# Kernel tuning notes

Hardware: AMD Instinct MI355X
Metric: run time of the kernel (lower is better)

## Reference

```python
import jax, jax.numpy as jnp
import numpy as np

NV, NH = 6000, 6000
DV, DH = 1024, 1024
HID, HEADS = 128, 3
EV, EH, EC = 200000, 200000, 32768


def _gat(x, ei, W, a_src, a_dst, bias, edge_attr=None, lin_e=None, a_e=None):
    """PyG GATConv (heads=H, concat=False, add_self_loops=True, LeakyReLU 0.2).
    Returns (node_out [N,C], alpha [E+N, H])."""
    N = x.shape[0]
    H, C = a_src.shape
    xw = (x @ W).reshape(N, H, C)                      # [N,H,C]
    asrc = jnp.einsum('nhc,hc->nh', xw, a_src)         # [N,H]
    adst = jnp.einsum('nhc,hc->nh', xw, a_dst)
    loop = jnp.arange(N, dtype=ei.dtype)               # self-loops appended
    src = jnp.concatenate([ei[0], loop])
    dst = jnp.concatenate([ei[1], loop])
    alpha = asrc[src] + adst[dst]                      # [E+N,H]
    if edge_attr is not None:
        # edge_dim=1 path: lin_edge(weight)[E,H,C] dotted with att_edge; self-loop attr = mean (PyG fill_value='mean')
        ea = jnp.concatenate([edge_attr, jnp.full((N,), jnp.mean(edge_attr), edge_attr.dtype)])
        ef = (ea[:, None] * lin_e[None, :]).reshape(-1, H, C)
        alpha = alpha + jnp.einsum('ehc,hc->eh', ef, a_e)
    alpha = jax.nn.leaky_relu(alpha, 0.2)
    # segment softmax over incoming edges of each destination node
    amax = jax.ops.segment_max(alpha, dst, num_segments=N)
    ex = jnp.exp(alpha - amax[dst])
    den = jax.ops.segment_sum(ex, dst, num_segments=N)
    alpha = ex / (den[dst] + 1e-16)
    out = jax.ops.segment_sum(xw[src] * alpha[..., None], dst, num_segments=N)
    return out.mean(axis=1) + bias, alpha              # concat=False -> head mean


def _bn(x, g, b):  # BatchNorm1d, training mode (batch stats, biased var)
    m = x.mean(0)
    v = x.var(0)
    return (x - m) / jnp.sqrt(v + 1e-5) * g + b


def reference(virus_data, host_data, coexistence_data, virus_edge_weight, host_edge_weight,
              vW, v_asrc, v_adst, v_bias, v_line, v_atte,
              hW, h_asrc, h_adst, h_bias, h_line, h_atte,
              vhW, vh_asrc, vh_adst, vh_bias,
              hvW, hv_asrc, hv_adst, hv_bias,
              linv_W, linv_b, linh_W, linh_b, bn_g, bn_b,
              virus_edge_index, host_edge_index, coexistence_edge_index, coexistence_edge_index_t):
    feat_v, alpha_v = _gat(virus_data, virus_edge_index, vW, v_asrc, v_adst, v_bias,
                           virus_edge_weight, v_line, v_atte)
    feat_h, alpha_h = _gat(host_data, host_edge_index, hW, h_asrc, h_adst, h_bias,
                           host_edge_weight, h_line, h_atte)
    feat_vh, alpha_vh = _gat(coexistence_data, coexistence_edge_index_t, vhW, vh_asrc, vh_adst, vh_bias)
    feat_hv, alpha_hv = _gat(coexistence_data.T, coexistence_edge_index, hvW, hv_asrc, hv_adst, hv_bias)

    vh = jax.nn.leaky_relu(_bn(virus_data @ linv_W + linv_b, bn_g, bn_b), 0.01)
    hh = jax.nn.leaky_relu(_bn(host_data @ linh_W + linh_b, bn_g, bn_b), 0.01)

    output_host = vh @ hh.T                  # [Nv,Nh]
    output_virus = (hh @ vh.T).T             # [Nv,Nh]
    return (output_host, output_virus, output_host + output_virus,
            alpha_v, alpha_h, alpha_vh, alpha_hv,
            feat_v, feat_h, feat_vh, feat_hv)


def setup_inputs() -> dict:
    key = jax.random.key(0)
    ks = iter(jax.random.split(key, 48))

    def nrm(shape, s=0.05):
        return (jax.random.normal(next(ks), shape, jnp.float32) * s).astype(jnp.float32)

    def gat_params(din, edge=True):
        p = [nrm((din, HEADS * HID)), nrm((HEADS, HID)), nrm((HEADS, HID)), jnp.zeros((HID,), jnp.float32)]
        if edge:
            p += [nrm((HEADS * HID,)), nrm((HEADS, HID))]
        return p

    inp = {
        'virus_data': jax.random.normal(next(ks), (NV, DV), jnp.float32),
        'host_data': jax.random.normal(next(ks), (NH, DH), jnp.float32),
        'coexistence_data': jax.random.normal(next(ks), (DV, DH), jnp.float32),
        'virus_edge_weight': jax.random.uniform(next(ks), (EV,), jnp.float32),
        'host_edge_weight': jax.random.uniform(next(ks), (EH,), jnp.float32),
    }
    for pref, din, edge in [('v', DV, True), ('h', DH, True)]:
        W, asrc, adst, b, le, ae = gat_params(din, True)
        inp.update({f'{pref}W': W, f'{pref}_asrc': asrc, f'{pref}_adst': adst,
                    f'{pref}_bias': b, f'{pref}_line': le, f'{pref}_atte': ae})
    for pref, din in [('vh', DH), ('hv', DV)]:
        W, asrc, adst, b = gat_params(din, False)
        inp.update({f'{pref}W': W, f'{pref}_asrc': asrc, f'{pref}_adst': adst, f'{pref}_bias': b})
    inp.update({
        'linv_W': nrm((DV, HID)), 'linv_b': jnp.zeros((HID,), jnp.float32),
        'linh_W': nrm((DH, HID)), 'linh_b': jnp.zeros((HID,), jnp.float32),
        'bn_g': jnp.ones((HID,), jnp.float32), 'bn_b': jnp.zeros((HID,), jnp.float32),
        'virus_edge_index': jax.random.randint(next(ks), (2, EV), 0, NV, jnp.int32),
        'host_edge_index': jax.random.randint(next(ks), (2, EH), 0, NH, jnp.int32),
        'coexistence_edge_index': jax.random.randint(next(ks), (2, EC), 0, DH, jnp.int32),
        'coexistence_edge_index_t': jax.random.randint(next(ks), (2, EC), 0, DV, jnp.int32),
    })
    return inp
```

## Files before the change

### kernel.cpp

```cpp
#include <hip/hip_runtime.h>

#define NV   6000
#define NH   6000
#define EV   200000
#define EH   200000
#define EC   32768
#define GCAP 256

typedef __attribute__((ext_vector_type(8))) short bf16x8;
typedef __attribute__((ext_vector_type(4))) float f32x4;

__device__ __forceinline__ unsigned short f2bf(float f){
  unsigned u = __float_as_uint(f);
  u += 0x7FFFu + ((u >> 16) & 1u);
  return (unsigned short)(u >> 16);
}
__device__ __forceinline__ float bf2f(unsigned short h){
  return __uint_as_float((unsigned)h << 16);
}

__global__ __launch_bounds__(256) void k_prep(
    const float* __restrict__ virus, const float* __restrict__ hostd, const float* __restrict__ coex,
    const float* __restrict__ vW, const float* __restrict__ linvW,
    const float* __restrict__ hW, const float* __restrict__ linhW,
    const float* __restrict__ vhW, const float* __restrict__ hvW,
    const float* __restrict__ v_as, const float* __restrict__ v_ad,
    const float* __restrict__ h_as, const float* __restrict__ h_ad,
    const float* __restrict__ vh_as, const float* __restrict__ vh_ad,
    const float* __restrict__ hv_as, const float* __restrict__ hv_ad,
    const float* __restrict__ vew, const float* __restrict__ hew,
    const float* __restrict__ v_line, const float* __restrict__ v_atte,
    const float* __restrict__ h_line, const float* __restrict__ h_atte,
    const int* __restrict__ vdst, const int* __restrict__ hdst,
    const int* __restrict__ c1dst, const int* __restrict__ c2dst,
    unsigned short* Avb, unsigned short* Ahb, unsigned short* Acb,
    unsigned short* Actb, unsigned short* BtV, unsigned short* BtH,
    unsigned short* BtVH, unsigned short* BtHV,
    float* WasV, float* WadV, float* WasH, float* WadH,
    float* WasC1, float* WadC1, float* WasC2, float* WadC2,
    float* sums, float* Kbuf,
    int* cntV, int* cntH, int* cntC1, int* cntC2)
{
  __shared__ float tp_lds[64][65];
  __shared__ float red4[4][2];
  int b = blockIdx.x, t = threadIdx.x;
  int lane = t & 63, w = t >> 6;

  if (b < 13024){
    int i = b * 256 + t;
    const float* src; unsigned short* dst; int off;
    if (i < 1536000)      { src = virus; dst = Avb; off = i; }
    else if (i < 3072000) { src = hostd; dst = Ahb; off = i - 1536000; }
    else                  { src = coex;  dst = Acb; off = i - 3072000; }
    float4 v = reinterpret_cast<const float4*>(src)[off];
    ushort4 o; o.x = f2bf(v.x); o.y = f2bf(v.y); o.z = f2bf(v.z); o.w = f2bf(v.w);
    reinterpret_cast<ushort4*>(dst)[off] = o;
    return;
  }
  b -= 13024;
  if (b < 704){
    const float* src; unsigned short* dst; int Nc, roff, ntn, rel;
    if      (b < 256){ src=coex;  dst=Actb; Nc=1024; roff=0;   ntn=16; rel=b; }
    else if (b < 352){ src=vW;    dst=BtV;  Nc=384;  roff=0;   ntn=6;  rel=b-256; }
    else if (b < 384){ src=linvW; dst=BtV;  Nc=128;  roff=384; ntn=2;  rel=b-352; }
    else if (b < 480){ src=hW;    dst=BtH;  Nc=384;  roff=0;   ntn=6;  rel=b-384; }
    else if (b < 512){ src=linhW; dst=BtH;  Nc=128;  roff=384; ntn=2;  rel=b-480; }
    else if (b < 608){ src=vhW;   dst=BtVH; Nc=384;  roff=0;   ntn=6;  rel=b-512; }
    else             { src=hvW;   dst=BtHV; Nc=384;  roff=0;   ntn=6;  rel=b-608; }
    int tn = rel % ntn, tk = rel / ntn;
    int k0 = tk * 64, n0 = tn * 64;
    int tx = t & 63, ty = t >> 6;
#pragma unroll
    for (int r = 0; r < 16; r++)
      tp_lds[ty + r*4][tx] = src[(size_t)(k0 + ty + r*4) * Nc + n0 + tx];
    __syncthreads();
#pragma unroll
    for (int r = 0; r < 16; r++)
      dst[(size_t)(n0 + ty + r*4 + roff) * 1024 + k0 + tx] = f2bf(tp_lds[tx][ty + r*4]);
    return;
  }
  b -= 704;
  if (b < 2048){
    int m = b >> 9;
    int krow = (b & 511) * 2 + (t >> 7);
    int c = t & 127;
    const float *W, *as_, *ad_; float *Was, *Wad;
    switch (m){
      case 0:  W=vW;  as_=v_as;  ad_=v_ad;  Was=WasV;  Wad=WadV;  break;
      case 1:  W=hW;  as_=h_as;  ad_=h_ad;  Was=WasH;  Wad=WadH;  break;
      case 2:  W=vhW; as_=vh_as; ad_=vh_ad; Was=WasC1; Wad=WadC1; break;
      default: W=hvW; as_=hv_as; ad_=hv_ad; Was=WasC2; Wad=WadC2; break;
    }
    const float* Wr = W + (size_t)krow * 384;
    for (int h = 0; h < 3; h++){
      float x = Wr[h*128 + c];
      float s = x * as_[h*128 + c], d = x * ad_[h*128 + c];
      for (int off = 32; off > 0; off >>= 1){ s += __shfl_down(s, off); d += __shfl_down(d, off); }
      if (lane == 0){ red4[w][0] = s; red4[w][1] = d; }
      __syncthreads();
      if (t == 0)  { Was[krow*3+h] = red4[0][0] + red4[1][0]; Wad[krow*3+h] = red4[0][1] + red4[1][1]; }
      if (t == 128){ Was[krow*3+h] = red4[2][0] + red4[3][0]; Wad[krow*3+h] = red4[2][1] + red4[3][1]; }
      __syncthreads();
    }
    return;
  }
  b -= 2048;
  if (b < 1819){
    int idx = b * 256 + t;
    if (idx >= EV + EH + 2*EC) return;
    const int* dp; int* cnt; int e;
    if      (idx < EV)       { dp=vdst;  cnt=cntV;  e=idx; }
    else if (idx < EV+EH)    { dp=hdst;  cnt=cntH;  e=idx-EV; }
    else if (idx < EV+EH+EC) { dp=c1dst; cnt=cntC1; e=idx-EV-EH; }
    else                     { dp=c2dst; cnt=cntC2; e=idx-EV-EH-EC; }
    atomicAdd(&cnt[dp[e]], 1);
    return;
  }
  b -= 1819;
  if (b < 256){
    int which = b >> 7, base = b & 127;
    const float* x = which ? hew : vew;
    float s = 0.f;
    for (int i = base*256 + t; i < EV; i += 128*256) s += x[i];
    for (int off = 32; off > 0; off >>= 1) s += __shfl_down(s, off);
    if (lane == 0) red4[w][0] = s;
    __syncthreads();
    if (t == 0) atomicAdd(&sums[which], red4[0][0]+red4[1][0]+red4[2][0]+red4[3][0]);
    return;
  }
  for (int h = 0; h < 3; h++){
    float s = (t < 128) ? v_line[h*128+t] * v_atte[h*128+t] : 0.f;
    for (int off = 32; off > 0; off >>= 1) s += __shfl_down(s, off);
    if (lane == 0) red4[w][0] = s;
    __syncthreads();
    if (t == 0) Kbuf[h] = red4[0][0]+red4[1][0]+red4[2][0]+red4[3][0];
    __syncthreads();
    s = (t < 128) ? h_line[h*128+t] * h_atte[h*128+t] : 0.f;
    for (int off = 32; off > 0; off >>= 1) s += __shfl_down(s, off);
    if (lane == 0) red4[w][0] = s;
    __syncthreads();
    if (t == 0) Kbuf[3+h] = red4[0][0]+red4[1][0]+red4[2][0]+red4[3][0];
    __syncthreads();
  }
}

__global__ __launch_bounds__(256) void k_nd(
    int* cntV, int* startsV, int* cntH, int* startsH,
    int* cntC1, int* startsC1, int* cntC2, int* startsC2,
    const float* __restrict__ virus, const float* __restrict__ hostd, const float* __restrict__ coex,
    const float* __restrict__ WasV, const float* __restrict__ WadV,
    const float* __restrict__ WasH, const float* __restrict__ WadH,
    const float* __restrict__ WasC1, const float* __restrict__ WadC1,
    const float* __restrict__ WasC2, const float* __restrict__ WadC2,
    float* asV, float* adV, float* asH, float* adH,
    float* asC1, float* adC1, float* asC2, float* adC2)
{
  __shared__ int   ssc[256];
  __shared__ float sh6[4][6];
  __shared__ float st[8][32][6];
  int b = blockIdx.x, t = threadIdx.x;

  if (b < 4){
    int* cnt; int* st_; int N;
    switch (b){
      case 0:  cnt=cntV;  st_=startsV;  N=NV;   break;
      case 1:  cnt=cntH;  st_=startsH;  N=NH;   break;
      case 2:  cnt=cntC1; st_=startsC1; N=1024; break;
      default: cnt=cntC2; st_=startsC2; N=1024; break;
    }
    int chunk = (N + 255) >> 8;
    int lo = t * chunk, hi = lo + chunk;
    if (hi > N) hi = N;
    if (lo > N) lo = N;
    int s = 0;
    for (int i = lo; i < hi; i++) s += cnt[i];
    ssc[t] = s;
    __syncthreads();
    for (int off = 1; off < 256; off <<= 1){
      int v = (t >= off) ? ssc[t - off] : 0;
      __syncthreads();
      ssc[t] += v;
      __syncthreads();
    }
    int run = ssc[t] - s;
    for (int i = lo; i < hi; i++){ st_[i] = run; run += cnt[i]; }
    if (t == 255) st_[N] = ssc[255];
    return;
  }
  b -= 4;
  if (b < 13024){
    const float *xb, *Was, *Wad; float *ao, *doo;
    if (b < 6000)       { xb=virus+(size_t)b*1024;        Was=WasV;  Wad=WadV;  ao=asV+b*3;          doo=adV+b*3; }
    else if (b < 12000) { int n=b-6000;  xb=hostd+(size_t)n*1024; Was=WasH;  Wad=WadH;  ao=asH+n*3;  doo=adH+n*3; }
    else                { int n=b-12000; xb=coex +(size_t)n*1024; Was=WasC1; Wad=WadC1; ao=asC1+n*3; doo=adC1+n*3; }
    float v[6] = {0,0,0,0,0,0};
    for (int k = t; k < 1024; k += 256){
      float xv = xb[k];
      v[0] += xv*Was[k*3+0]; v[1] += xv*Was[k*3+1]; v[2] += xv*Was[k*3+2];
      v[3] += xv*Wad[k*3+0]; v[4] += xv*Wad[k*3+1]; v[5] += xv*Wad[k*3+2];
    }
    int lane = t & 63, w = t >> 6;
    for (int off = 32; off > 0; off >>= 1)
#pragma unroll
      for (int i = 0; i < 6; i++) v[i] += __shfl_down(v[i], off);
    if (lane == 0)
#pragma unroll
      for (int i = 0; i < 6; i++) sh6[w][i] = v[i];
    __syncthreads();
    if (t < 6){
      float r = sh6[0][t] + sh6[1][t] + sh6[2][t] + sh6[3][t];
      if (t < 3) ao[t] = r; else doo[t-3] = r;
    }
    return;
  }
  b -= 13024;
  int c = t & 31, ks = t >> 5;
  int nn = b * 32 + c;
  float a[6] = {0,0,0,0,0,0};
  for (int k = ks*128; k < ks*128 + 128; k++){
    float xv = coex[(size_t)k*1024 + nn];
    a[0] += xv*WasC2[k*3+0]; a[1] += xv*WasC2[k*3+1]; a[2] += xv*WasC2[k*3+2];
    a[3] += xv*WadC2[k*3+0]; a[4] += xv*WadC2[k*3+1]; a[5] += xv*WadC2[k*3+2];
  }
#pragma unroll
  for (int j = 0; j < 6; j++) st[ks][c][j] = a[j];
  __syncthreads();
  if (t < 32){
    float r[6] = {0,0,0,0,0,0};
#pragma unroll
    for (int k = 0; k < 8; k++)
#pragma unroll
      for (int j = 0; j < 6; j++) r[j] += st[k][t][j];
    int n2 = b * 32 + t;
    asC2[n2*3] = r[0]; asC2[n2*3+1] = r[1]; asC2[n2*3+2] = r[2];
    adC2[n2*3] = r[3]; adC2[n2*3+1] = r[4]; adC2[n2*3+2] = r[5];
  }
}

template<int MODE>
__device__ __forceinline__ void gemm_body(
    const unsigned short* __restrict__ A, const unsigned short* __restrict__ B,
    int M, int N, unsigned short* __restrict__ xwb, float* __restrict__ lin,
    int bx, int by)
{
  const int tid  = threadIdx.x;
  const int lane = tid & 63, w = tid >> 6;
  const int wr = w >> 1, wc = w & 1;
  const int R  = by * 128 + wr * 64;
  const int Cb = bx * 128 + wc * 64;
  const int r0 = lane & 15, kg = lane >> 4;

  const unsigned short* pa[4]; const unsigned short* pb[4];
  bool va[4], vb[4];
#pragma unroll
  for (int i = 0; i < 4; i++){
    int row = R + i * 16 + r0;
    va[i] = row < M;
    pa[i] = A + (size_t)(va[i] ? row : 0) * 1024 + kg * 8;
    int col = Cb + i * 16 + r0;
    vb[i] = col < N;
    pb[i] = B + (size_t)(vb[i] ? col : 0) * 1024 + kg * 8;
  }
  const bf16x8 Z8 = {0,0,0,0,0,0,0,0};
  f32x4 acc[4][4];
#pragma unroll
  for (int i = 0; i < 4; i++)
#pragma unroll
    for (int j = 0; j < 4; j++) acc[i][j] = (f32x4){0.f,0.f,0.f,0.f};

  for (int kk = 0; kk < 1024; kk += 32){
    bf16x8 av[4], bv[4];
#pragma unroll
    for (int i = 0; i < 4; i++){
      bf16x8 ta = *reinterpret_cast<const bf16x8*>(pa[i] + kk);
      bf16x8 tb = *reinterpret_cast<const bf16x8*>(pb[i] + kk);
      av[i] = va[i] ? ta : Z8;
      bv[i] = vb[i] ? tb : Z8;
    }
#pragma unroll
    for (int i = 0; i < 4; i++)
#pragma unroll
      for (int j = 0; j < 4; j++)
        acc[i][j] = __builtin_amdgcn_mfma_f32_16x16x32_bf16(av[i], bv[j], acc[i][j], 0, 0, 0);
  }

  const int cn = lane & 15, rq = (lane >> 4) * 4;
#pragma unroll
  for (int i = 0; i < 4; i++){
    int row0 = R + i * 16 + rq;
#pragma unroll
    for (int j = 0; j < 4; j++){
      int col = Cb + j * 16 + cn;
      if (col < N){
#pragma unroll
        for (int r = 0; r < 4; r++){
          int row = row0 + r;
          if (row < M){
            float v = acc[i][j][r];
            if (MODE == 0){
              if (col < 384) xwb[(size_t)row * 384 + col] = f2bf(v);
              else           lin[(size_t)row * 128 + col - 384] = v;
            } else {
              xwb[(size_t)row * 384 + col] = f2bf(v);
            }
          }
        }
      }
    }
  }
}

__global__ __launch_bounds__(256) void k_sg(
    const unsigned short* Avb, const unsigned short* BtV, unsigned short* xwbV, float* linV,
    const unsigned short* Ahb, const unsigned short* BtH, unsigned short* xwbH, float* linH,
    const unsigned short* Acb,  const unsigned short* BtVH, unsigned short* xwbC1,
    const unsigned short* Actb, const unsigned short* BtHV, unsigned short* xwbC2,
    const int* vdst, const int* hdst, const int* c1dst, const int* c2dst,
    const int* stV, const int* stH, const int* st1, const int* st2,
    int* cuV, int* cuH, int* cu1, int* cu2,
    int* soV, int* soH, int* so1, int* so2)
{
  int b = blockIdx.x;
  if (b < 424){
    if (b < 188)      gemm_body<0>(Avb,  BtV,  NV,   512, xwbV,  linV, b & 3, b >> 2);
    else if (b < 376){ int g = b - 188; gemm_body<0>(Ahb,  BtH,  NH,   512, xwbH,  linH, g & 3, g >> 2); }
    else if (b < 400){ int g = b - 376; gemm_body<1>(Acb,  BtVH, 1024, 384, xwbC1, nullptr, g % 3, g / 3); }
    else             { int g = b - 400; gemm_body<1>(Actb, BtHV, 1024, 384, xwbC2, nullptr, g % 3, g / 3); }
    return;
  }
  int idx = (b - 424) * 256 + threadIdx.x;
  if (idx >= EV + EH + 2*EC) return;
  const int* dp; const int* st; int* cur; int* so; int e;
  if      (idx < EV)       { dp=vdst;  st=stV; cur=cuV; so=soV; e=idx; }
  else if (idx < EV+EH)    { dp=hdst;  st=stH; cur=cuH; so=soH; e=idx-EV; }
  else if (idx < EV+EH+EC) { dp=c1dst; st=st1; cur=cu1; so=so1; e=idx-EV-EH; }
  else                     { dp=c2dst; st=st2; cur=cu2; so=so2; e=idx-EV-EH-EC; }
  int d = dp[e];
  so[st[d] + atomicAdd(&cur[d], 1)] = e;
}

struct GatDesc {
  const unsigned short* xwb; const int* src; const int* sorted; const int* starts;
  const float* as_; const float* ad_; const float* Kc; const float* ew; const float* sumw;
  const float* bias; float* alpha; float* feat;
  int E; float invE;
};

__global__ __launch_bounds__(256) void k_gatbn(
    GatDesc dV, GatDesc dH, GatDesc d1, GatDesc d2,
    const float* __restrict__ linV, const float* __restrict__ linH, float* __restrict__ bnacc)
{
  int b = blockIdx.x, t = threadIdx.x;
  if (b >= 14048){
    int bb = b - 14048;
    int which = bb >= 188;
    int r0 = (which ? bb - 188 : bb) * 32 + (t >> 7) * 16;
    int c = t & 127;
    const float* lin = which ? linH : linV;
    float s = 0.f, q = 0.f;
#pragma unroll
    for (int r = 0; r < 16; r++){
      int row = r0 + r;
      if (row < NV){
        float v = lin[(size_t)row * 128 + c];
        s += v; q += v * v;
      }
    }
    atomicAdd(&bnacc[which*256 + c],       s);
    atomicAdd(&bnacc[which*256 + 128 + c], q);
    return;
  }
  GatDesc d; int n;
  if (b < 6000)       { d = dV; n = b; }
  else if (b < 12000) { d = dH; n = b - 6000; }
  else if (b < 13024) { d = d1; n = b - 12000; }
  else                { d = d2; n = b - 13024; }

  const int lane = t & 63, w = t >> 6;
  const int c = t & 127, half = t >> 7;
  __shared__ float shx[GCAP][3];
  __shared__ int   shs[GCAP];
  __shared__ float redm[4][3], reds[4][3], shD[128][3];

  const int s0  = d.starts[n];
  const int deg = d.starts[n+1] - s0;
  const bool hasW = (d.ew != nullptr);
  float K0=0.f, K1=0.f, K2=0.f, wself=0.f;
  if (hasW){ K0=d.Kc[0]; K1=d.Kc[1]; K2=d.Kc[2]; wself = d.sumw[0] * d.invE; }
  const float ad0 = d.ad_[n*3], ad1 = d.ad_[n*3+1], ad2 = d.ad_[n*3+2];
  float sr0 = d.as_[n*3+0] + ad0 + wself*K0;  sr0 = sr0 >= 0.f ? sr0 : 0.2f*sr0;
  float sr1 = d.as_[n*3+1] + ad1 + wself*K1;  sr1 = sr1 >= 0.f ? sr1 : 0.2f*sr1;
  float sr2 = d.as_[n*3+2] + ad2 + wself*K2;  sr2 = sr2 >= 0.f ? sr2 : 0.2f*sr2;

  float mx0 = sr0, mx1 = sr1, mx2 = sr2;
  for (int i = t; i < deg; i += 256){
    int e = d.sorted[s0 + i];
    int s = d.src[e];
    float wv = hasW ? d.ew[e] : 0.f;
    float r0 = d.as_[s*3+0] + ad0 + wv*K0;  r0 = r0 >= 0.f ? r0 : 0.2f*r0;
    float r1 = d.as_[s*3+1] + ad1 + wv*K1;  r1 = r1 >= 0.f ? r1 : 0.2f*r1;
    float r2 = d.as_[s*3+2] + ad2 + wv*K2;  r2 = r2 >= 0.f ? r2 : 0.2f*r2;
    if (i < GCAP){ shs[i] = s; shx[i][0]=r0; shx[i][1]=r1; shx[i][2]=r2; }
    mx0 = fmaxf(mx0, r0); mx1 = fmaxf(mx1, r1); mx2 = fmaxf(mx2, r2);
  }
  for (int off = 32; off > 0; off >>= 1){
    mx0 = fmaxf(mx0, __shfl_down(mx0, off));
    mx1 = fmaxf(mx1, __shfl_down(mx1, off));
    mx2 = fmaxf(mx2, __shfl_down(mx2, off));
  }
  if (lane == 0){ redm[w][0]=mx0; redm[w][1]=mx1; redm[w][2]=mx2; }
  __syncthreads();
  const float M0 = fmaxf(fmaxf(redm[0][0],redm[1][0]), fmaxf(redm[2][0],redm[3][0]));
  const float M1 = fmaxf(fmaxf(redm[0][1],redm[1][1]), fmaxf(redm[2][1],redm[3][1]));
  const float M2 = fmaxf(fmaxf(redm[0][2],redm[1][2]), fmaxf(redm[2][2],redm[3][2]));

  float t0 = 0.f, t1 = 0.f, t2 = 0.f;
  for (int i = t; i < deg; i += 256){
    float r0, r1, r2;
    if (i < GCAP){ r0 = shx[i][0]; r1 = shx[i][1]; r2 = shx[i][2]; }
    else {
      int e = d.sorted[s0 + i]; int s = d.src[e];
      float wv = hasW ? d.ew[e] : 0.f;
      r0 = d.as_[s*3+0]+ad0+wv*K0; r0 = r0>=0.f?r0:0.2f*r0;
      r1 = d.as_[s*3+1]+ad1+wv*K1; r1 = r1>=0.f?r1:0.2f*r1;
      r2 = d.as_[s*3+2]+ad2+wv*K2; r2 = r2>=0.f?r2:0.2f*r2;
    }
    float e0 = expf(r0 - M0), e1 = expf(r1 - M1), e2 = expf(r2 - M2);
    if (i < GCAP){ shx[i][0]=e0; shx[i][1]=e1; shx[i][2]=e2; }
    t0 += e0; t1 += e1; t2 += e2;
  }
  for (int off = 32; off > 0; off >>= 1){
    t0 += __shfl_down(t0, off); t1 += __shfl_down(t1, off); t2 += __shfl_down(t2, off);
  }
  if (lane == 0){ reds[w][0]=t0; reds[w][1]=t1; reds[w][2]=t2; }
  __syncthreads();
  const float se0 = expf(sr0 - M0), se1 = expf(sr1 - M1), se2 = expf(sr2 - M2);
  const float i0 = 1.f / (reds[0][0]+reds[1][0]+reds[2][0]+reds[3][0] + se0 + 1e-16f);
  const float i1 = 1.f / (reds[0][1]+reds[1][1]+reds[2][1]+reds[3][1] + se1 + 1e-16f);
  const float i2 = 1.f / (reds[0][2]+reds[1][2]+reds[2][2]+reds[3][2] + se2 + 1e-16f);

  for (int i = t; i < deg; i += 256){
    int e = d.sorted[s0 + i];
    float e0, e1, e2;
    if (i < GCAP){ e0 = shx[i][0]; e1 = shx[i][1]; e2 = shx[i][2]; }
    else {
      int s = d.src[e];
      float wv = hasW ? d.ew[e] : 0.f;
      float r0 = d.as_[s*3+0]+ad0+wv*K0; r0=r0>=0.f?r0:0.2f*r0;
      float r1 = d.as_[s*3+1]+ad1+wv*K1; r1=r1>=0.f?r1:0.2f*r1;
      float r2 = d.as_[s*3+2]+ad2+wv*K2; r2=r2>=0.f?r2:0.2f*r2;
      e0 = expf(r0-M0); e1 = expf(r1-M1); e2 = expf(r2-M2);
    }
    float* ap = d.alpha + (size_t)e * 3;
    ap[0] = e0 * i0; ap[1] = e1 * i1; ap[2] = e2 * i2;
  }
  if (t == 0){
    float* ap = d.alpha + (size_t)(d.E + n) * 3;
    ap[0] = se0 * i0; ap[1] = se1 * i1; ap[2] = se2 * i2;
  }

  float f0, f1, f2;
  if (half == 0){
    const unsigned short* xn = d.xwb + (size_t)n * 384;
    f0 = bf2f(xn[c]) * se0; f1 = bf2f(xn[128+c]) * se1; f2 = bf2f(xn[256+c]) * se2;
  } else { f0 = f1 = f2 = 0.f; }
  for (int i = half; i < deg; i += 2){
    int s; float e0, e1, e2;
    if (i < GCAP){ s = shs[i]; e0 = shx[i][0]; e1 = shx[i][1]; e2 = shx[i][2]; }
    else {
      int e = d.sorted[s0 + i]; s = d.src[e];
      float wv = hasW ? d.ew[e] : 0.f;
      float r0 = d.as_[s*3+0]+ad0+wv*K0; r0=r0>=0.f?r0:0.2f*r0;
      float r1 = d.as_[s*3+1]+ad1+wv*K1; r1=r1>=0.f?r1:0.2f*r1;
      float r2 = d.as_[s*3+2]+ad2+wv*K2; r2=r2>=0.f?r2:0.2f*r2;
      e0 = expf(r0-M0); e1 = expf(r1-M1); e2 = expf(r2-M2);
    }
    const unsigned short* xs = d.xwb + (size_t)s * 384;
    f0 += bf2f(xs[c]) * e0; f1 += bf2f(xs[128+c]) * e1; f2 += bf2f(xs[256+c]) * e2;
  }
  if (half == 1){ shD[c][0] = f0; shD[c][1] = f1; shD[c][2] = f2; }
  __syncthreads();
  if (half == 0){
    f0 += shD[c][0]; f1 += shD[c][1]; f2 += shD[c][2];
    d.feat[(size_t)n*128 + c] = (f0*i0 + f1*i1 + f2*i2) * (1.f/3.f) + d.bias[c];
  }
}

__global__ __launch_bounds__(256) void k_fin(
    const float* __restrict__ linV, const float* __restrict__ linH,
    const float* __restrict__ bnacc, const float* __restrict__ g, const float* __restrict__ bb,
    float* __restrict__ o0, float* __restrict__ o1, float* __restrict__ o2)
{
  __shared__ float sA[128], hA[128], sB[128], hB[128];
  const int t = threadIdx.x;
  if (t < 128){
    float mu  = bnacc[t] * (1.f/NV);
    float var = bnacc[128+t] * (1.f/NV) - mu*mu;
    float rs  = rsqrtf(var + 1e-5f);
    sA[t] = rs * g[t]; hA[t] = bb[t] - mu * rs * g[t];
  } else {
    int j = t - 128;
    float mu  = bnacc[256+j] * (1.f/NV);
    float var = bnacc[384+j] * (1.f/NV) - mu*mu;
    float rs  = rsqrtf(var + 1e-5f);
    sB[j] = rs * g[j]; hB[j] = bb[j] - mu * rs * g[j];
  }
  __syncthreads();

  const int lane = t & 63, w = t >> 6;
  const int wr = w >> 1, wc = w & 1;
  const int R  = blockIdx.y * 128 + wr * 64;
  const int Cb = blockIdx.x * 128 + wc * 64;
  const int r0 = lane & 15, kg = lane >> 4;

  const float* pa[4]; const float* pb[4];
  bool va[4], vb[4];
#pragma unroll
  for (int i = 0; i < 4; i++){
    int row = R + i * 16 + r0;
    va[i] = row < NV;
    pa[i] = linV + (size_t)(va[i] ? row : 0) * 128 + kg * 8;
    int col = Cb + i * 16 + r0;
    vb[i] = col < NH;
    pb[i] = linH + (size_t)(vb[i] ? col : 0) * 128 + kg * 8;
  }
  const bf16x8 Z8 = {0,0,0,0,0,0,0,0};
  f32x4 acc[4][4];
#pragma unroll
  for (int i = 0; i < 4; i++)
#pragma unroll
    for (int j = 0; j < 4; j++) acc[i][j] = (f32x4){0.f,0.f,0.f,0.f};

  for (int kk = 0; kk < 128; kk += 32){
    const int kb = kk + kg * 8;
    bf16x8 av[4], bv[4];
#pragma unroll
    for (int i = 0; i < 4; i++){
      bf16x8 fa, fb;
#pragma unroll
      for (int e = 0; e < 8; e++){
        float v1 = fmaf(pa[i][kk + e], sA[kb + e], hA[kb + e]);
        v1 = v1 >= 0.f ? v1 : 0.01f * v1;
        fa[e] = (short)f2bf(v1);
        float v2 = fmaf(pb[i][kk + e], sB[kb + e], hB[kb + e]);
        v2 = v2 >= 0.f ? v2 : 0.01f * v2;
        fb[e] = (short)f2bf(v2);
      }
      av[i] = va[i] ? fa : Z8;
      bv[i] = vb[i] ? fb : Z8;
    }
#pragma unroll
    for (int i = 0; i < 4; i++)
#pragma unroll
      for (int j = 0; j < 4; j++)
        acc[i][j] = __builtin_amdgcn_mfma_f32_16x16x32_bf16(av[i], bv[j], acc[i][j], 0, 0, 0);
  }

  const int cn = lane & 15, rq = (lane >> 4) * 4;
#pragma unroll
  for (int i = 0; i < 4; i++){
    int row0 = R + i * 16 + rq;
#pragma unroll
    for (int j = 0; j < 4; j++){
      int col = Cb + j * 16 + cn;
      if (col < NH){
#pragma unroll
        for (int r = 0; r < 4; r++){
          int row = row0 + r;
          if (row < NV){
            size_t idx = (size_t)row * NH + col;
            float v = acc[i][j][r];
            o0[idx] = v; o1[idx] = v; o2[idx] = v + v;
          }
        }
      }
    }
  }
}

extern "C" void kernel_launch(void* const* d_in, const int* in_sizes, int n_in,
                              void* d_out, int out_size, void* d_ws, size_t ws_size,
                              hipStream_t stream)
{
  (void)in_sizes; (void)n_in; (void)out_size; (void)ws_size;
  const float* virus  = (const float*)d_in[0];
  const float* hostd  = (const float*)d_in[1];
  const float* coex   = (const float*)d_in[2];
  const float* vew    = (const float*)d_in[3];
  const float* hew    = (const float*)d_in[4];
  const float* vW     = (const float*)d_in[5];
  const float* v_as   = (const float*)d_in[6];
  const float* v_ad   = (const float*)d_in[7];
  const float* v_bias = (const float*)d_in[8];
  const float* v_line = (const float*)d_in[9];
  const float* v_atte = (const float*)d_in[10];
  const float* hW     = (const float*)d_in[11];
  const float* h_as   = (const float*)d_in[12];
  const float* h_ad   = (const float*)d_in[13];
  const float* h_bias = (const float*)d_in[14];
  const float* h_line = (const float*)d_in[15];
  const float* h_atte = (const float*)d_in[16];
  const float* vhW    = (const float*)d_in[17];
  const float* vh_as  = (const float*)d_in[18];
  const float* vh_ad  = (const float*)d_in[19];
  const float* vh_bias= (const float*)d_in[20];
  const float* hvW    = (const float*)d_in[21];
  const float* hv_as  = (const float*)d_in[22];
  const float* hv_ad  = (const float*)d_in[23];
  const float* hv_bias= (const float*)d_in[24];
  const float* linvW  = (const float*)d_in[25];
  const float* linhW  = (const float*)d_in[27];
  const float* bng    = (const float*)d_in[29];
  const float* bnb    = (const float*)d_in[30];
  const int* vei  = (const int*)d_in[31];
  const int* hei  = (const int*)d_in[32];
  const int* cei  = (const int*)d_in[33];
  const int* ceit = (const int*)d_in[34];

  float* out = (float*)d_out;
  float* o0 = out;
  float* o1 = out + 36000000ll;
  float* o2 = out + 72000000ll;
  float* alpha_v  = out + 108000000ll;
  float* alpha_h  = alpha_v  + 618000;
  float* alpha_vh = alpha_h  + 618000;
  float* alpha_hv = alpha_vh + 101376;
  float* feat_v   = alpha_hv + 101376;
  float* feat_h   = feat_v   + 768000;
  float* feat_vh  = feat_h   + 768000;
  float* feat_hv  = feat_vh  + 131072;

  char* wp = (char*)d_ws;
  auto alloc = [&](size_t b) -> void* { void* p = wp; wp += (b + 255) & ~(size_t)255; return p; };
  unsigned short* Avb  = (unsigned short*)alloc((size_t)NV*1024*2);
  unsigned short* Ahb  = (unsigned short*)alloc((size_t)NH*1024*2);
  unsigned short* Acb  = (unsigned short*)alloc((size_t)1024*1024*2);
  unsigned short* Actb = (unsigned short*)alloc((size_t)1024*1024*2);
  unsigned short* BtV  = (unsigned short*)alloc((size_t)512*1024*2);
  unsigned short* BtH  = (unsigned short*)alloc((size_t)512*1024*2);
  unsigned short* BtVH = (unsigned short*)alloc((size_t)384*1024*2);
  unsigned short* BtHV = (unsigned short*)alloc((size_t)384*1024*2);
  unsigned short* xwbV = (unsigned short*)alloc((size_t)NV*384*2);
  unsigned short* xwbH = (unsigned short*)alloc((size_t)NH*384*2);
  unsigned short* xwbC1= (unsigned short*)alloc((size_t)1024*384*2);
  unsigned short* xwbC2= (unsigned short*)alloc((size_t)1024*384*2);
  float* linV = (float*)alloc((size_t)NV*128*4);
  float* linH = (float*)alloc((size_t)NH*128*4);
  float* asV  = (float*)alloc(NV*3*4);   float* adV  = (float*)alloc(NV*3*4);
  float* asH  = (float*)alloc(NH*3*4);   float* adH  = (float*)alloc(NH*3*4);
  float* asC1 = (float*)alloc(1024*3*4); float* adC1 = (float*)alloc(1024*3*4);
  float* asC2 = (float*)alloc(1024*3*4); float* adC2 = (float*)alloc(1024*3*4);
  float* WasV = (float*)alloc(1024*3*4); float* WadV = (float*)alloc(1024*3*4);
  float* WasH = (float*)alloc(1024*3*4); float* WadH = (float*)alloc(1024*3*4);
  float* WasC1= (float*)alloc(1024*3*4); float* WadC1= (float*)alloc(1024*3*4);
  float* WasC2= (float*)alloc(1024*3*4); float* WadC2= (float*)alloc(1024*3*4);
  int* startsV  = (int*)alloc((NV+1)*4);  int* sortedV  = (int*)alloc((size_t)EV*4);
  int* startsH  = (int*)alloc((NH+1)*4);  int* sortedH  = (int*)alloc((size_t)EH*4);
  int* startsC1 = (int*)alloc(1025*4);    int* sortedC1 = (int*)alloc((size_t)EC*4);
  int* startsC2 = (int*)alloc(1025*4);    int* sortedC2 = (int*)alloc((size_t)EC*4);
  float* Kbuf  = (float*)alloc(256);
  char* z0 = wp;
  int* cntV  = (int*)alloc(NV*4);   int* curV  = (int*)alloc(NV*4);
  int* cntH  = (int*)alloc(NH*4);   int* curH  = (int*)alloc(NH*4);
  int* cntC1 = (int*)alloc(1024*4); int* curC1 = (int*)alloc(1024*4);
  int* cntC2 = (int*)alloc(1024*4); int* curC2 = (int*)alloc(1024*4);
  float* sums  = (float*)alloc(256);
  float* bnacc = (float*)alloc(512*4);
  hipMemsetAsync(z0, 0, (size_t)(wp - z0), stream);

  const int* vsrc = vei,  *vdst = vei  + EV;
  const int* hsrc = hei,  *hdst = hei  + EH;
  const int* c1src= ceit, *c1dst= ceit + EC;
  const int* c2src= cei,  *c2dst= cei  + EC;

  k_prep<<<17852, 256, 0, stream>>>(virus, hostd, coex,
      vW, linvW, hW, linhW, vhW, hvW,
      v_as, v_ad, h_as, h_ad, vh_as, vh_ad, hv_as, hv_ad,
      vew, hew, v_line, v_atte, h_line, h_atte,
      vdst, hdst, c1dst, c2dst,
      Avb, Ahb, Acb, Actb, BtV, BtH, BtVH, BtHV,
      WasV, WadV, WasH, WadH, WasC1, WadC1, WasC2, WadC2,
      sums, Kbuf, cntV, cntH, cntC1, cntC2);
  k_nd<<<13060, 256, 0, stream>>>(cntV, startsV, cntH, startsH, cntC1, startsC1, cntC2, startsC2,
      virus, hostd, coex,
      WasV, WadV, WasH, WadH, WasC1, WadC1, WasC2, WadC2,
      asV, adV, asH, adH, asC1, adC1, asC2, adC2);
  k_sg<<<2243, 256, 0, stream>>>(Avb, BtV, xwbV, linV, Ahb, BtH, xwbH, linH,
      Acb, BtVH, xwbC1, Actb, BtHV, xwbC2,
      vdst, hdst, c1dst, c2dst,
      startsV, startsH, startsC1, startsC2,
      curV, curH, curC1, curC2,
      sortedV, sortedH, sortedC1, sortedC2);
  {
    GatDesc dv = { xwbV,  vsrc,  sortedV,  startsV,  asV,  adV,  Kbuf,   vew, &sums[0], v_bias,
                   alpha_v,  feat_v,  EV, 1.f/EV };
    GatDesc dh = { xwbH,  hsrc,  sortedH,  startsH,  asH,  adH,  Kbuf+3, hew, &sums[1], h_bias,
                   alpha_h,  feat_h,  EH, 1.f/EH };
    GatDesc dc1= { xwbC1, c1src, sortedC1, startsC1, asC1, adC1, nullptr, nullptr, nullptr, vh_bias,
                   alpha_vh, feat_vh, EC, 0.f };
    GatDesc dc2= { xwbC2, c2src, sortedC2, startsC2, asC2, adC2, nullptr, nullptr, nullptr, hv_bias,
                   alpha_hv, feat_hv, EC, 0.f };
    k_gatbn<<<14424, 256, 0, stream>>>(dv, dh, dc1, dc2, linV, linH, bnacc);
  }
  k_fin<<<dim3(47,47), 256, 0, stream>>>(linV, linH, bnacc, bng, bnb, o0, o1, o2);
}
```

Baseline: 835.9 us.

## Fuse bf16 conversion with attention-score projection and halve GEMM column tile

The fp32-to-bf16 conversion of the virus, host and coexistence rows now happens in the same block that computes the per-node attention source and destination dot products. Each input row is read once instead of twice, and the old k_prep is split so the weight-derived vectors are computed first in a small kernel. The GEMM per-block column tile shrinks from 128 to 64, which doubles the GEMM block count to improve occupancy and load balance at the cost of reloading the A operand more often. The prefix-scan and transposes move into the merged kernel.

Measured after the change: 837.3 us. About the same (+0.2%).

```diff
diff --git a/kernel.cpp b/kernel.cpp
--- a/kernel.cpp
+++ b/kernel.cpp
@@ -19,67 +19,25 @@
   return __uint_as_float((unsigned)h << 16);
 }
 
-__global__ __launch_bounds__(256) void k_prep(
-    const float* __restrict__ virus, const float* __restrict__ hostd, const float* __restrict__ coex,
-    const float* __restrict__ vW, const float* __restrict__ linvW,
-    const float* __restrict__ hW, const float* __restrict__ linhW,
-    const float* __restrict__ vhW, const float* __restrict__ hvW,
-    const float* __restrict__ v_as, const float* __restrict__ v_ad,
-    const float* __restrict__ h_as, const float* __restrict__ h_ad,
-    const float* __restrict__ vh_as, const float* __restrict__ vh_ad,
-    const float* __restrict__ hv_as, const float* __restrict__ hv_ad,
+__global__ __launch_bounds__(256) void k0(
+    const float* __restrict__ vW, const float* __restrict__ v_as, const float* __restrict__ v_ad,
+    const float* __restrict__ hW, const float* __restrict__ h_as, const float* __restrict__ h_ad,
+    const float* __restrict__ vhW, const float* __restrict__ vh_as, const float* __restrict__ vh_ad,
+    const float* __restrict__ hvW, const float* __restrict__ hv_as, const float* __restrict__ hv_ad,
     const float* __restrict__ vew, const float* __restrict__ hew,
     const float* __restrict__ v_line, const float* __restrict__ v_atte,
     const float* __restrict__ h_line, const float* __restrict__ h_atte,
     const int* __restrict__ vdst, const int* __restrict__ hdst,
     const int* __restrict__ c1dst, const int* __restrict__ c2dst,
-    unsigned short* Avb, unsigned short* Ahb, unsigned short* Acb,
-    unsigned short* Actb, unsigned short* BtV, unsigned short* BtH,
-    unsigned short* BtVH, unsigned short* BtHV,
     float* WasV, float* WadV, float* WasH, float* WadH,
     float* WasC1, float* WadC1, float* WasC2, float* WadC2,
     float* sums, float* Kbuf,
     int* cntV, int* cntH, int* cntC1, int* cntC2)
 {
-  __shared__ float tp_lds[64][65];
   __shared__ float red4[4][2];
   int b = blockIdx.x, t = threadIdx.x;
   int lane = t & 63, w = t >> 6;
 
-  if (b < 13024){
-    int i = b * 256 + t;
-    const float* src; unsigned short* dst; int off;
-    if (i < 1536000)      { src = virus; dst = Avb; off = i; }
-    else if (i < 3072000) { src = hostd; dst = Ahb; off = i - 1536000; }
-    else                  { src = coex;  dst = Acb; off = i - 3072000; }
-    float4 v = reinterpret_cast<const float4*>(src)[off];
-    ushort4 o; o.x = f2bf(v.x); o.y = f2bf(v.y); o.z = f2bf(v.z); o.w = f2bf(v.w);
-    reinterpret_cast<ushort4*>(dst)[off] = o;
-    return;
-  }
-  b -= 13024;
-  if (b < 704){
-    const float* src; unsigned short* dst; int Nc, roff, ntn, rel;
-    if      (b < 256){ src=coex;  dst=Actb; Nc=1024; roff=0;   ntn=16; rel=b; }
-    else if (b < 352){ src=vW;    dst=BtV;  Nc=384;  roff=0;   ntn=6;  rel=b-256; }
-    else if (b < 384){ src=linvW; dst=BtV;  Nc=128;  roff=384; ntn=2;  rel=b-352; }
-    else if (b < 480){ src=hW;    dst=BtH;  Nc=384;  roff=0;   ntn=6;  rel=b-384; }
-    else if (b < 512){ src=linhW; dst=BtH;  Nc=128;  roff=384; ntn=2;  rel=b-480; }
-    else if (b < 608){ src=vhW;   dst=BtVH; Nc=384;  roff=0;   ntn=6;  rel=b-512; }
-    else             { src=hvW;   dst=BtHV; Nc=384;  roff=0;   ntn=6;  rel=b-608; }
-    int tn = rel % ntn, tk = rel / ntn;
-    int k0 = tk * 64, n0 = tn * 64;
-    int tx = t & 63, ty = t >> 6;
-#pragma unroll
-    for (int r = 0; r < 16; r++)
-      tp_lds[ty + r*4][tx] = src[(size_t)(k0 + ty + r*4) * Nc + n0 + tx];
-    __syncthreads();
-#pragma unroll
-    for (int r = 0; r < 16; r++)
-      dst[(size_t)(n0 + ty + r*4 + roff) * 1024 + k0 + tx] = f2bf(tp_lds[tx][ty + r*4]);
-    return;
-  }
-  b -= 704;
   if (b < 2048){
     int m = b >> 9;
     int krow = (b & 511) * 2 + (t >> 7);
@@ -144,97 +102,136 @@
   }
 }
 
-__global__ __launch_bounds__(256) void k_nd(
-    int* cntV, int* startsV, int* cntH, int* startsH,
-    int* cntC1, int* startsC1, int* cntC2, int* startsC2,
+__global__ __launch_bounds__(256) void k_prep(
     const float* __restrict__ virus, const float* __restrict__ hostd, const float* __restrict__ coex,
+    const float* __restrict__ vW, const float* __restrict__ linvW,
+    const float* __restrict__ hW, const float* __restrict__ linhW,
+    const float* __restrict__ vhW, const float* __restrict__ hvW,
     const float* __restrict__ WasV, const float* __restrict__ WadV,
     const float* __restrict__ WasH, const float* __restrict__ WadH,
     const float* __restrict__ WasC1, const float* __restrict__ WadC1,
     const float* __restrict__ WasC2, const float* __restrict__ WadC2,
+    int* cntV, int* startsV, int* cntH, int* startsH,
+    int* cntC1, int* startsC1, int* cntC2, int* startsC2,
+    unsigned short* Avb, unsigned short* Ahb, unsigned short* Acb,
+    unsigned short* Actb, unsigned short* BtV, unsigned short* BtH,
+    unsigned short* BtVH, unsigned short* BtHV,
     float* asV, float* adV, float* asH, float* adH,
     float* asC1, float* adC1, float* asC2, float* adC2)
 {
-  __shared__ int   ssc[256];
-  __shared__ float sh6[4][6];
-  __shared__ float st[8][32][6];
+  __shared__ float scratch[64*65];
   int b = blockIdx.x, t = threadIdx.x;
-
-  if (b < 4){
-    int* cnt; int* st_; int N;
-    switch (b){
-      case 0:  cnt=cntV;  st_=startsV;  N=NV;   break;
-      case 1:  cnt=cntH;  st_=startsH;  N=NH;   break;
-      case 2:  cnt=cntC1; st_=startsC1; N=1024; break;
-      default: cnt=cntC2; st_=startsC2; N=1024; break;
-    }
-    int chunk = (N + 255) >> 8;
-    int lo = t * chunk, hi = lo + chunk;
-    if (hi > N) hi = N;
-    if (lo > N) lo = N;
-    int s = 0;
-    for (int i = lo; i < hi; i++) s += cnt[i];
-    ssc[t] = s;
-    __syncthreads();
-    for (int off = 1; off < 256; off <<= 1){
-      int v = (t >= off) ? ssc[t - off] : 0;
-      __syncthreads();
-      ssc[t] += v;
-      __syncthreads();
-    }
-    int run = ssc[t] - s;
-    for (int i = lo; i < hi; i++){ st_[i] = run; run += cnt[i]; }
-    if (t == 255) st_[N] = ssc[255];
+  int lane = t & 63, w = t >> 6;
+
+  if (b < 13024){
+    const float* x; unsigned short* dstp; const float* Was; const float* Wad;
+    float* ao; float* doo; int row;
+    if (b < 6000)       { row=b;       x=virus; dstp=Avb; Was=WasV;  Wad=WadV;  ao=asV;  doo=adV; }
+    else if (b < 12000) { row=b-6000;  x=hostd; dstp=Ahb; Was=WasH;  Wad=WadH;  ao=asH;  doo=adH; }
+    else                { row=b-12000; x=coex;  dstp=Acb; Was=WasC1; Wad=WadC1; ao=asC1; doo=adC1; }
+    float4 v = reinterpret_cast<const float4*>(x + (size_t)row * 1024)[t];
+    ushort4 o; o.x = f2bf(v.x); o.y = f2bf(v.y); o.z = f2bf(v.z); o.w = f2bf(v.w);
+    reinterpret_cast<ushort4*>(dstp + (size_t)row * 1024)[t] = o;
+    const float4* Wp = reinterpret_cast<const float4*>(Was + t*12);
+    float4 wa = Wp[0], wb = Wp[1], wcc = Wp[2];
+    const float4* Dp = reinterpret_cast<const float4*>(Wad + t*12);
+    float4 da = Dp[0], db = Dp[1], dcc = Dp[2];
+    float r[6];
+    r[0] = v.x*wa.x + v.y*wa.w + v.z*wb.z + v.w*wcc.y;
+    r[1] = v.x*wa.y + v.y*wb.x + v.z*wb.w + v.w*wcc.z;
+    r[2] = v.x*wa.z + v.y*wb.y + v.z*wcc.x + v.w*wcc.w;
+    r[3] = v.x*da.x + v.y*da.w + v.z*db.z + v.w*dcc.y;
+    r[4] = v.x*da.y + v.y*db.x + v.z*db.w + v.w*dcc.z;
+    r[5] = v.x*da.z + v.y*db.y + v.z*dcc.x + v.w*dcc.w;
+    for (int off = 32; off > 0; off >>= 1)
+#pragma unroll
+      for (int i = 0; i < 6; i++) r[i] += __shfl_down(r[i], off);
+    float (*sh6)[6] = (float(*)[6])scratch;
+    if (lane == 0)
+#pragma unroll
+      for (int i = 0; i < 6; i++) sh6[w][i] = r[i];
+    __syncthreads();
+    if (t < 6){
+      float s = sh6[0][t] + sh6[1][t] + sh6[2][t] + sh6[3][t];
+      if (t < 3) ao[row*3 + t] = s; else doo[row*3 + (t-3)] = s;
+    }
     return;
   }
-  b -= 4;
-  if (b < 13024){
-    const float *xb, *Was, *Wad; float *ao, *doo;
-    if (b < 6000)       { xb=virus+(size_t)b*1024;        Was=WasV;  Wad=WadV;  ao=asV+b*3;          doo=adV+b*3; }
-    else if (b < 12000) { int n=b-6000;  xb=hostd+(size_t)n*1024; Was=WasH;  Wad=WadH;  ao=asH+n*3;  doo=adH+n*3; }
-    else                { int n=b-12000; xb=coex +(size_t)n*1024; Was=WasC1; Wad=WadC1; ao=asC1+n*3; doo=adC1+n*3; }
-    float v[6] = {0,0,0,0,0,0};
-    for (int k = t; k < 1024; k += 256){
-      float xv = xb[k];
-      v[0] += xv*Was[k*3+0]; v[1] += xv*Was[k*3+1]; v[2] += xv*Was[k*3+2];
-      v[3] += xv*Wad[k*3+0]; v[4] += xv*Wad[k*3+1]; v[5] += xv*Wad[k*3+2];
-    }
-    int lane = t & 63, w = t >> 6;
-    for (int off = 32; off > 0; off >>= 1)
-#pragma unroll
-      for (int i = 0; i < 6; i++) v[i] += __shfl_down(v[i], off);
-    if (lane == 0)
-#pragma unroll
-      for (int i = 0; i < 6; i++) sh6[w][i] = v[i];
-    __syncthreads();
-    if (t < 6){
-      float r = sh6[0][t] + sh6[1][t] + sh6[2][t] + sh6[3][t];
-      if (t < 3) ao[t] = r; else doo[t-3] = r;
-    }
+  b -= 13024;
+  if (b < 704){
+    float (*tp_lds)[65] = (float(*)[65])scratch;
+    const float* src; unsigned short* dst; int Nc, roff, ntn, rel;
+    if      (b < 256){ src=coex;  dst=Actb; Nc=1024; roff=0;   ntn=16; rel=b; }
+    else if (b < 352){ src=vW;    dst=BtV;  Nc=384;  roff=0;   ntn=6;  rel=b-256; }
+    else if (b < 384){ src=linvW; dst=BtV;  Nc=128;  roff=384; ntn=2;  rel=b-352; }
+    else if (b < 480){ src=hW;    dst=BtH;  Nc=384;  roff=0;   ntn=6;  rel=b-384; }
+    else if (b < 512){ src=linhW; dst=BtH;  Nc=128;  roff=384; ntn=2;  rel=b-480; }
+    else if (b < 608){ src=vhW;   dst=BtVH; Nc=384;  roff=0;   ntn=6;  rel=b-512; }
+    else             { src=hvW;   dst=BtHV; Nc=384;  roff=0;   ntn=6;  rel=b-608; }
+    int tn = rel % ntn, tk = rel / ntn;
+    int k0_ = tk * 64, n0 = tn * 64;
+    int tx = t & 63, ty = t >> 6;
+#pragma unroll
+    for (int r = 0; r < 16; r++)
+      tp_lds[ty + r*4][tx] = src[(size_t)(k0_ + ty + r*4) * Nc + n0 + tx];
+    __syncthreads();
+#pragma unroll
+    for (int r = 0; r < 16; r++)
+      dst[(size_t)(n0 + ty + r*4 + roff) * 1024 + k0_ + tx] = f2bf(tp_lds[tx][ty + r*4]);
     return;
   }
-  b -= 13024;
-  int c = t & 31, ks = t >> 5;
-  int nn = b * 32 + c;
-  float a[6] = {0,0,0,0,0,0};
-  for (int k = ks*128; k < ks*128 + 128; k++){
-    float xv = coex[(size_t)k*1024 + nn];
-    a[0] += xv*WasC2[k*3+0]; a[1] += xv*WasC2[k*3+1]; a[2] += xv*WasC2[k*3+2];
-    a[3] += xv*WadC2[k*3+0]; a[4] += xv*WadC2[k*3+1]; a[5] += xv*WadC2[k*3+2];
-  }
-#pragma unroll
-  for (int j = 0; j < 6; j++) st[ks][c][j] = a[j];
+  b -= 704;
+  if (b < 32){
+    float (*st)[32][6] = (float(*)[32][6])scratch;
+    int c = t & 31, ks = t >> 5;
+    int nn = b * 32 + c;
+    float a[6] = {0,0,0,0,0,0};
+    for (int k = ks*128; k < ks*128 + 128; k++){
+      float xv = coex[(size_t)k*1024 + nn];
+      a[0] += xv*WasC2[k*3+0]; a[1] += xv*WasC2[k*3+1]; a[2] += xv*WasC2[k*3+2];
+      a[3] += xv*WadC2[k*3+0]; a[4] += xv*WadC2[k*3+1]; a[5] += xv*WadC2[k*3+2];
+    }
+#pragma unroll
+    for (int j = 0; j < 6; j++) st[ks][c][j] = a[j];
+    __syncthreads();
+    if (t < 32){
+      float r[6] = {0,0,0,0,0,0};
+#pragma unroll
+      for (int k = 0; k < 8; k++)
+#pragma unroll
+        for (int j = 0; j < 6; j++) r[j] += st[k][t][j];
+      int n2 = b * 32 + t;
+      asC2[n2*3] = r[0]; asC2[n2*3+1] = r[1]; asC2[n2*3+2] = r[2];
+      adC2[n2*3] = r[3]; adC2[n2*3+1] = r[4]; adC2[n2*3+2] = r[5];
+    }
+    return;
+  }
+  b -= 32;
+  int* ssc = (int*)scratch;
+  int* cnt; int* st_; int N;
+  switch (b){
+    case 0:  cnt=cntV;  st_=startsV;  N=NV;   break;
+    case 1:  cnt=cntH;  st_=startsH;  N=NH;   break;
+    case 2:  cnt=cntC1; st_=startsC1; N=1024; break;
+    default: cnt=cntC2; st_=startsC2; N=1024; break;
+  }
+  int chunk = (N + 255) >> 8;
+  int lo = t * chunk, hi = lo + chunk;
+  if (hi > N) hi = N;
+  if (lo > N) lo = N;
+  int s = 0;
+  for (int i = lo; i < hi; i++) s += cnt[i];
+  ssc[t] = s;
   __syncthreads();
-  if (t < 32){
-    float r[6] = {0,0,0,0,0,0};
-#pragma unroll
-    for (int k = 0; k < 8; k++)
-#pragma unroll
-      for (int j = 0; j < 6; j++) r[j] += st[k][t][j];
-    int n2 = b * 32 + t;
-    asC2[n2*3] = r[0]; asC2[n2*3+1] = r[1]; asC2[n2*3+2] = r[2];
-    adC2[n2*3] = r[3]; adC2[n2*3+1] = r[4]; adC2[n2*3+2] = r[5];
-  }
+  for (int off = 1; off < 256; off <<= 1){
+    int v = (t >= off) ? ssc[t - off] : 0;
+    __syncthreads();
+    ssc[t] += v;
+    __syncthreads();
+  }
+  int run = ssc[t] - s;
+  for (int i = lo; i < hi; i++){ st_[i] = run; run += cnt[i]; }
+  if (t == 255) st_[N] = ssc[255];
 }
 
 template<int MODE>
@@ -247,40 +244,46 @@
   const int lane = tid & 63, w = tid >> 6;
   const int wr = w >> 1, wc = w & 1;
   const int R  = by * 128 + wr * 64;
-  const int Cb = bx * 128 + wc * 64;
+  const int Cb = bx * 64 + wc * 32;
   const int r0 = lane & 15, kg = lane >> 4;
 
-  const unsigned short* pa[4]; const unsigned short* pb[4];
-  bool va[4], vb[4];
+  const unsigned short* pa[4]; const unsigned short* pb[2];
+  bool va[4], vb[2];
 #pragma unroll
   for (int i = 0; i < 4; i++){
     int row = R + i * 16 + r0;
     va[i] = row < M;
     pa[i] = A + (size_t)(va[i] ? row : 0) * 1024 + kg * 8;
-    int col = Cb + i * 16 + r0;
-    vb[i] = col < N;
-    pb[i] = B + (size_t)(vb[i] ? col : 0) * 1024 + kg * 8;
+  }
+#pragma unroll
+  for (int j = 0; j < 2; j++){
+    int col = Cb + j * 16 + r0;
+    vb[j] = col < N;
+    pb[j] = B + (size_t)(vb[j] ? col : 0) * 1024 + kg * 8;
   }
   const bf16x8 Z8 = {0,0,0,0,0,0,0,0};
-  f32x4 acc[4][4];
+  f32x4 acc[4][2];
 #pragma unroll
   for (int i = 0; i < 4; i++)
 #pragma unroll
-    for (int j = 0; j < 4; j++) acc[i][j] = (f32x4){0.f,0.f,0.f,0.f};
+    for (int j = 0; j < 2; j++) acc[i][j] = (f32x4){0.f,0.f,0.f,0.f};
 
   for (int kk = 0; kk < 1024; kk += 32){
-    bf16x8 av[4], bv[4];
+    bf16x8 av[4], bv[2];
 #pragma unroll
     for (int i = 0; i < 4; i++){
       bf16x8 ta = *reinterpret_cast<const bf16x8*>(pa[i] + kk);
-      bf16x8 tb = *reinterpret_cast<const bf16x8*>(pb[i] + kk);
       av[i] = va[i] ? ta : Z8;
-      bv[i] = vb[i] ? tb : Z8;
+    }
+#pragma unroll
+    for (int j = 0; j < 2; j++){
+      bf16x8 tb = *reinterpret_cast<const bf16x8*>(pb[j] + kk);
+      bv[j] = vb[j] ? tb : Z8;
     }
 #pragma unroll
     for (int i = 0; i < 4; i++)
 #pragma unroll
-      for (int j = 0; j < 4; j++)
+      for (int j = 0; j < 2; j++)
         acc[i][j] = __builtin_amdgcn_mfma_f32_16x16x32_bf16(av[i], bv[j], acc[i][j], 0, 0, 0);
   }
 
@@ -289,7 +292,7 @@
   for (int i = 0; i < 4; i++){
     int row0 = R + i * 16 + rq;
 #pragma unroll
-    for (int j = 0; j < 4; j++){
+    for (int j = 0; j < 2; j++){
       int col = Cb + j * 16 + cn;
       if (col < N){
 #pragma unroll
@@ -321,14 +324,14 @@
     int* soV, int* soH, int* so1, int* so2)
 {
   int b = blockIdx.x;
-  if (b < 424){
-    if (b < 188)      gemm_body<0>(Avb,  BtV,  NV,   512, xwbV,  linV, b & 3, b >> 2);
-    else if (b < 376){ int g = b - 188; gemm_body<0>(Ahb,  BtH,  NH,   512, xwbH,  linH, g & 3, g >> 2); }
-    else if (b < 400){ int g = b - 376; gemm_body<1>(Acb,  BtVH, 1024, 384, xwbC1, nullptr, g % 3, g / 3); }
-    else             { int g = b - 400; gemm_body<1>(Actb, BtHV, 1024, 384, xwbC2, nullptr, g % 3, g / 3); }
+  if (b < 848){
+    if (b < 376)       gemm_body<0>(Avb,  BtV,  NV,   512, xwbV,  linV, b & 7, b >> 3);
+    else if (b < 752){ int g = b - 376; gemm_body<0>(Ahb,  BtH,  NH,   512, xwbH,  linH, g & 7, g >> 3); }
+    else if (b < 800){ int g = b - 752; gemm_body<1>(Acb,  BtVH, 1024, 384, xwbC1, nullptr, g % 6, g / 6); }
+    else             { int g = b - 800; gemm_body<1>(Actb, BtHV, 1024, 384, xwbC2, nullptr, g % 6, g / 6); }
     return;
   }
-  int idx = (b - 424) * 256 + threadIdx.x;
+  int idx = (b - 848) * 256 + threadIdx.x;
   if (idx >= EV + EH + 2*EC) return;
   const int* dp; const int* st; int* cur; int* so; int e;
   if      (idx < EV)       { dp=vdst;  st=stV; cur=cuV; so=soV; e=idx; }
@@ -673,19 +676,19 @@
   const int* c1src= ceit, *c1dst= ceit + EC;
   const int* c2src= cei,  *c2dst= cei  + EC;
 
-  k_prep<<<17852, 256, 0, stream>>>(virus, hostd, coex,
-      vW, linvW, hW, linhW, vhW, hvW,
-      v_as, v_ad, h_as, h_ad, vh_as, vh_ad, hv_as, hv_ad,
+  k0<<<4124, 256, 0, stream>>>(vW, v_as, v_ad, hW, h_as, h_ad,
+      vhW, vh_as, vh_ad, hvW, hv_as, hv_ad,
       vew, hew, v_line, v_atte, h_line, h_atte,
       vdst, hdst, c1dst, c2dst,
-      Avb, Ahb, Acb, Actb, BtV, BtH, BtVH, BtHV,
       WasV, WadV, WasH, WadH, WasC1, WadC1, WasC2, WadC2,
       sums, Kbuf, cntV, cntH, cntC1, cntC2);
-  k_nd<<<13060, 256, 0, stream>>>(cntV, startsV, cntH, startsH, cntC1, startsC1, cntC2, startsC2,
-      virus, hostd, coex,
+  k_prep<<<13764, 256, 0, stream>>>(virus, hostd, coex,
+      vW, linvW, hW, linhW, vhW, hvW,
       WasV, WadV, WasH, WadH, WasC1, WadC1, WasC2, WadC2,
+      cntV, startsV, cntH, startsH, cntC1, startsC1, cntC2, startsC2,
+      Avb, Ahb, Acb, Actb, BtV, BtH, BtVH, BtHV,
       asV, adV, asH, adH, asC1, adC1, asC2, adC2);
-  k_sg<<<2243, 256, 0, stream>>>(Avb, BtV, xwbV, linV, Ahb, BtH, xwbH, linH,
+  k_sg<<<2667, 256, 0, stream>>>(Avb, BtV, xwbV, linV, Ahb, BtH, xwbH, linH,
       Acb, BtVH, xwbC1, Actb, BtHV, xwbC2,
       vdst, hdst, c1dst, c2dst,
       startsV, startsH, startsC1, startsC2,
```
